# Kernel tuning notes

Measured on AMD Instinct MI355X. Metric: run time of the kernel, lower is better.

Reference implementation:

```python
import math
import jax, jax.numpy as jnp
import numpy as np

B, D, N, K = 16, 512, 2048, 32  # batch, latent_dim, n points, k feature width


def setup_inputs() -> dict:
    key = jax.random.key(0)
    ks = jax.random.split(key, 11)
    s = 0.02
    return {
        "x": jax.random.normal(ks[0], (B, D), jnp.float32),
        "WQ": jax.random.normal(ks[1], (D, N * K), jnp.float32) * s,
        "bQ": jax.random.normal(ks[2], (N * K,), jnp.float32) * s,
        "WK": jax.random.normal(ks[3], (D, N * K), jnp.float32) * s,
        "bK": jax.random.normal(ks[4], (N * K,), jnp.float32) * s,
        "WV": jax.random.normal(ks[5], (D, N * K), jnp.float32) * s,
        "bV": jax.random.normal(ks[6], (N * K,), jnp.float32) * s,
        "Wout": jax.random.normal(ks[7], (3, K), jnp.float32) * s,
        "bout": jax.random.normal(ks[8], (3,), jnp.float32) * s,
        "Wori": jax.random.normal(ks[9], (3, K), jnp.float32) * s,
        "bori": jax.random.normal(ks[10], (3,), jnp.float32) * s,
    }


def reference(x, WQ, bQ, WK, bK, WV, bV, Wout, bout, Wori, bori):
    b = x.shape[0]
    q = (x @ WQ + bQ).reshape(b, N, K)   # fc_Q output, used for both Q and ori
    k = (x @ WK + bK).reshape(b, N, K)
    v = (x @ WV + bV).reshape(b, N, K)
    # conv_ori is a pointwise Conv1d(K, 3, 1) applied to ori^T -> [b,3,N];
    # computed in [b,N,3] layout (final output layout after the last transpose).
    ori = jnp.einsum('bnk,ck->bnc', q, Wori) + bori  # [b, N, 3]
    # single-head scaled dot-product attention, scores [b, N, N]
    scores = jnp.einsum('bnk,bmk->bnm', q, k) / math.sqrt(K)
    attn = jax.nn.softmax(scores, axis=2)
    out = jnp.einsum('bnm,bmk->bnk', attn, v)        # [b, N, K]
    out = jnp.einsum('bnk,ck->bnc', out, Wout) + bout  # pointwise conv_output
    return out + ori                                 # [b, N, 3]
```

## Files before the change

kernel.cpp:

```cpp
#include <hip/hip_runtime.h>
#include <hip/hip_bf16.h>
#include <math.h>

#define NB 16
#define ND 512
#define NN 2048
#define NKF 32
#define NNK 65536

typedef short s8v __attribute__((ext_vector_type(8)));
typedef float f4v __attribute__((ext_vector_type(4)));
typedef unsigned short u16;
typedef unsigned int u32;
typedef u16 u16x8 __attribute__((ext_vector_type(8)));
typedef u32 u32x4 __attribute__((ext_vector_type(4)));

__device__ __forceinline__ u16 f2bf(float x) {
    u32 u = __builtin_bit_cast(u32, x);
    return (u16)((u + 0x7fffu + ((u >> 16) & 1u)) >> 16);
}
__device__ __forceinline__ float bf2f(u16 b) {
    u32 u = ((u32)b) << 16;
    return __builtin_bit_cast(float, u);
}

__global__ __launch_bounds__(256) void proj_partial(
    const float* __restrict__ x,
    const float* __restrict__ WQ, const float* __restrict__ WK,
    const float* __restrict__ WV, u16* __restrict__ part)
{
    const int t = threadIdx.x;
    const int jb = blockIdx.x;
    const int mat = blockIdx.y;
    const int dz = blockIdx.z;
    const float* __restrict__ W = (mat == 0) ? WQ : (mat == 1) ? WK : WV;
    const int j = jb * 1024 + t * 4;
    const int d0 = dz * 128;

    f4v acc[16];
    #pragma unroll
    for (int b = 0; b < 16; b++) acc[b] = (f4v){0.f, 0.f, 0.f, 0.f};

    const float* wp = W + (size_t)d0 * NNK + j;
    const float* xp = x + d0;

    f4v wa[8], wb[8];
    #pragma unroll
    for (int u = 0; u < 8; u++)
        wa[u] = __builtin_nontemporal_load((const f4v*)(wp + (size_t)u * NNK));

    #pragma unroll 1
    for (int dd = 0; dd < 128; dd += 16) {
        #pragma unroll
        for (int u = 0; u < 8; u++)
            wb[u] = __builtin_nontemporal_load(
                (const f4v*)(wp + (size_t)(dd + 8 + u) * NNK));
        __builtin_amdgcn_sched_barrier(0);

        #pragma unroll
        for (int u = 0; u < 8; u++) {
            const float* xr = xp + dd + u;
            #pragma unroll
            for (int b = 0; b < 16; b++) {
                float xv = xr[b * ND];
                acc[b][0] = fmaf(xv, wa[u][0], acc[b][0]);
                acc[b][1] = fmaf(xv, wa[u][1], acc[b][1]);
                acc[b][2] = fmaf(xv, wa[u][2], acc[b][2]);
                acc[b][3] = fmaf(xv, wa[u][3], acc[b][3]);
            }
        }

        if (dd + 16 < 128) {
            #pragma unroll
            for (int u = 0; u < 8; u++)
                wa[u] = __builtin_nontemporal_load(
                    (const f4v*)(wp + (size_t)(dd + 16 + u) * NNK));
        }
        __builtin_amdgcn_sched_barrier(0);

        #pragma unroll
        for (int u = 0; u < 8; u++) {
            const float* xr = xp + dd + 8 + u;
            #pragma unroll
            for (int b = 0; b < 16; b++) {
                float xv = xr[b * ND];
                acc[b][0] = fmaf(xv, wb[u][0], acc[b][0]);
                acc[b][1] = fmaf(xv, wb[u][1], acc[b][1]);
                acc[b][2] = fmaf(xv, wb[u][2], acc[b][2]);
                acc[b][3] = fmaf(xv, wb[u][3], acc[b][3]);
            }
        }
    }

    size_t base = ((size_t)(mat * 4 + dz) * 16) * NNK + j;
    #pragma unroll
    for (int b = 0; b < 16; b++) {
        u32 lo = (u32)f2bf(acc[b][0]) | ((u32)f2bf(acc[b][1]) << 16);
        u32 hi = (u32)f2bf(acc[b][2]) | ((u32)f2bf(acc[b][3]) << 16);
        *(uint2*)(part + base + (size_t)b * NNK) = make_uint2(lo, hi);
    }
}

__global__ __launch_bounds__(256) void reduce_cast(
    const u16* __restrict__ part,
    const float* __restrict__ bQ, const float* __restrict__ bK,
    const float* __restrict__ bV,
    u16* __restrict__ qb, u16* __restrict__ kb, u16* __restrict__ vT)
{
    const int t = threadIdx.x;
    const int jc = blockIdx.x;
    const int b  = blockIdx.y;
    const int mat = blockIdx.z;
    const float* __restrict__ bias = (mat == 0) ? bQ : (mat == 1) ? bK : bV;
    const int j = jc * 2048 + t * 8;

    float4 b0 = *(const float4*)(bias + j);
    float4 b1 = *(const float4*)(bias + j + 4);
    float v[8] = {b0.x, b0.y, b0.z, b0.w, b1.x, b1.y, b1.z, b1.w};

    #pragma unroll
    for (int dz = 0; dz < 4; dz++) {
        size_t p = ((size_t)(mat * 4 + dz) * 16 + b) * NNK + j;
        u16x8 pp = *(const u16x8*)(part + p);
        #pragma unroll
        for (int i = 0; i < 8; i++) v[i] += bf2f(pp[i]);
    }

    const float scale = (mat == 1) ? 0.2550868230023389f : 1.0f;
    u16 h[8];
    #pragma unroll
    for (int i = 0; i < 8; i++) h[i] = f2bf(v[i] * scale);

    __shared__ u16 vt[32][72];

    if (mat < 2) {
        u16* dst = ((mat == 0) ? qb : kb) + (size_t)b * NNK + j;
        u16x8 hv;
        #pragma unroll
        for (int i = 0; i < 8; i++) hv[i] = h[i];
        *(u16x8*)dst = hv;
    } else {
        const int n  = t >> 2;
        const int k0 = (t & 3) * 8;
        #pragma unroll
        for (int i = 0; i < 8; i++) vt[k0 + i][n] = h[i];
        __syncthreads();
        const int k  = t >> 3;
        const int c8 = t & 7;
        u16x8 ov;
        #pragma unroll
        for (int i = 0; i < 8; i++) ov[i] = vt[k][c8 * 8 + i];
        u16* dst = vT + (size_t)b * NNK + (size_t)k * NN + jc * 64 + c8 * 8;
        *(u16x8*)dst = ov;
    }
}

__global__ __launch_bounds__(256) void attn_kernel(
    const u16* __restrict__ qb, const u16* __restrict__ kb,
    const u16* __restrict__ vT,
    const float* __restrict__ Wout, const float* __restrict__ bout,
    const float* __restrict__ Wori, const float* __restrict__ bori,
    float* __restrict__ out)
{
    const int t = threadIdx.x;
    const int w = t >> 6;
    const int l = t & 63;
    const int g = l >> 4;
    const int n = l & 15;
    const int b = blockIdx.y;
    const int q0 = blockIdx.x * 64;

    __shared__ __align__(16) u16 Ks[2][2048];
    __shared__ __align__(16) u16 Vs[2][2048];

    const u16* qrow = qb + (size_t)b * NNK + (size_t)(q0 + w * 16 + n) * NKF + g * 8;
    const s8v qf = *(const s8v*)qrow;

    const int krow = t >> 2, kcol = (t & 3) * 8;
    const int vrow = t >> 3, vslot = t & 7;
    const int vcolL = (vslot ^ (vrow & 7)) * 8;
    const u16* kgp = kb + (size_t)b * NNK + (size_t)krow * NKF + kcol;
    const u16* vgp = vT + (size_t)b * NNK + (size_t)vrow * NN + vcolL;

    s8v kreg, vreg;
    kreg = *(const s8v*)(kgp);                 vreg = *(const s8v*)(vgp);
    *(s8v*)(&Ks[0][t * 8]) = kreg;             *(s8v*)(&Vs[0][t * 8]) = vreg;
    kreg = *(const s8v*)(kgp + (size_t)2048);  vreg = *(const s8v*)(vgp + 64);
    __syncthreads();

    float m_run = -INFINITY, l_run = 0.f;
    f4v O0 = {0.f, 0.f, 0.f, 0.f}, O1 = {0.f, 0.f, 0.f, 0.f};
    const bool hi = (l >= 32);
    const int srcA = ((2 * g) & 3) * 16 + n;
    const int srcB = ((2 * g + 1) & 3) * 16 + n;

    for (int it = 0; it < 32; it++) {
        const int cur = it & 1;
        if (it + 1 < 32) {
            *(s8v*)(&Ks[cur ^ 1][t * 8]) = kreg;
            *(s8v*)(&Vs[cur ^ 1][t * 8]) = vreg;
        }
        if (it + 2 < 32) {
            kreg = *(const s8v*)(kgp + (size_t)(it + 2) * 2048);
            vreg = *(const s8v*)(vgp + (size_t)(it + 2) * 64);
        }

        f4v S[4];
        #pragma unroll
        for (int tt = 0; tt < 4; tt++) {
            s8v ka = *(const s8v*)(&Ks[cur][(n + 16 * tt) * NKF + g * 8]);
            f4v z = {0.f, 0.f, 0.f, 0.f};
            S[tt] = __builtin_amdgcn_mfma_f32_16x16x32_bf16(ka, qf, z, 0, 0, 0);
        }

        float pmax = -INFINITY;
        #pragma unroll
        for (int tt = 0; tt < 4; tt++)
            #pragma unroll
            for (int r = 0; r < 4; r++) pmax = fmaxf(pmax, S[tt][r]);
        pmax = fmaxf(pmax, __shfl_xor(pmax, 16));
        pmax = fmaxf(pmax, __shfl_xor(pmax, 32));
        const float m_new = fmaxf(m_run, pmax);
        const float corr = exp2f(m_run - m_new);

        float p[4][4];
        float tsum = 0.f;
        #pragma unroll
        for (int tt = 0; tt < 4; tt++)
            #pragma unroll
            for (int r = 0; r < 4; r++) {
                p[tt][r] = exp2f(S[tt][r] - m_new);
                tsum += p[tt][r];
            }
        tsum += __shfl_xor(tsum, 16);
        tsum += __shfl_xor(tsum, 32);
        l_run = l_run * corr + tsum;
        m_run = m_new;
        #pragma unroll
        for (int r = 0; r < 4; r++) { O0[r] *= corr; O1[r] *= corr; }

        u32 pk[4][2];
        #pragma unroll
        for (int tt = 0; tt < 4; tt++) {
            pk[tt][0] = (u32)f2bf(p[tt][0]) | ((u32)f2bf(p[tt][1]) << 16);
            pk[tt][1] = (u32)f2bf(p[tt][2]) | ((u32)f2bf(p[tt][3]) << 16);
        }

        #pragma unroll
        for (int kc = 0; kc < 2; kc++) {
            u32 lo0 = (u32)__shfl((int)pk[2 * kc][0], srcA);
            u32 hi0 = (u32)__shfl((int)pk[2 * kc + 1][0], srcA);
            u32 lo1 = (u32)__shfl((int)pk[2 * kc][1], srcA);
            u32 hi1 = (u32)__shfl((int)pk[2 * kc + 1][1], srcA);
            u32 lo2 = (u32)__shfl((int)pk[2 * kc][0], srcB);
            u32 hi2 = (u32)__shfl((int)pk[2 * kc + 1][0], srcB);
            u32 lo3 = (u32)__shfl((int)pk[2 * kc][1], srcB);
            u32 hi3 = (u32)__shfl((int)pk[2 * kc + 1][1], srcB);
            u32x4 fr;
            fr.x = hi ? hi0 : lo0;
            fr.y = hi ? hi1 : lo1;
            fr.z = hi ? hi2 : lo2;
            fr.w = hi ? hi3 : lo3;
            s8v pa = __builtin_bit_cast(s8v, fr);

            {
                int row = n;
                int slot = (g + 4 * kc) ^ (row & 7);
                s8v va = *(const s8v*)(&Vs[cur][row * 64 + slot * 8]);
                O0 = __builtin_amdgcn_mfma_f32_16x16x32_bf16(va, pa, O0, 0, 0, 0);
            }
            {
                int row = n + 16;
                int slot = (g + 4 * kc) ^ (row & 7);
                s8v va = *(const s8v*)(&Vs[cur][row * 64 + slot * 8]);
                O1 = __builtin_amdgcn_mfma_f32_16x16x32_bf16(va, pa, O1, 0, 0, 0);
            }
        }
        __syncthreads();
    }

    const float inv = 1.0f / l_run;
    float po[3] = {0.f, 0.f, 0.f};
    #pragma unroll
    for (int r = 0; r < 4; r++) {
        int dk0 = 4 * g + r;
        int dk1 = 16 + 4 * g + r;
        float o0 = O0[r] * inv;
        float o1 = O1[r] * inv;
        #pragma unroll
        for (int c = 0; c < 3; c++) {
            po[c] += o0 * Wout[c * NKF + dk0];
            po[c] += o1 * Wout[c * NKF + dk1];
        }
    }
    #pragma unroll
    for (int e = 0; e < 8; e++) {
        float qv = bf2f((u16)qf[e]);
        int k = 8 * g + e;
        #pragma unroll
        for (int c = 0; c < 3; c++) po[c] += qv * Wori[c * NKF + k];
    }
    #pragma unroll
    for (int c = 0; c < 3; c++) {
        po[c] += __shfl_xor(po[c], 16);
        po[c] += __shfl_xor(po[c], 32);
    }
    if (g == 0) {
        int row = q0 + w * 16 + n;
        size_t o = ((size_t)b * NN + row) * 3;
        #pragma unroll
        for (int c = 0; c < 3; c++) out[o + c] = po[c] + bout[c] + bori[c];
    }
}

extern "C" void kernel_launch(void* const* d_in, const int* in_sizes, int n_in,
                              void* d_out, int out_size, void* d_ws, size_t ws_size,
                              hipStream_t stream) {
    const float* x    = (const float*)d_in[0];
    const float* WQ   = (const float*)d_in[1];
    const float* bQ   = (const float*)d_in[2];
    const float* WK   = (const float*)d_in[3];
    const float* bK   = (const float*)d_in[4];
    const float* WV   = (const float*)d_in[5];
    const float* bV   = (const float*)d_in[6];
    const float* Wout = (const float*)d_in[7];
    const float* bout = (const float*)d_in[8];
    const float* Wori = (const float*)d_in[9];
    const float* bori = (const float*)d_in[10];
    float* out = (float*)d_out;

    char* ws = (char*)d_ws;
    u16* part = (u16*)ws;
    u16* qb = (u16*)(ws + 25165824);
    u16* kb = (u16*)(ws + 25165824 + 2097152);
    u16* vT = (u16*)(ws + 25165824 + 2 * 2097152);

    proj_partial<<<dim3(64, 3, 4), 256, 0, stream>>>(x, WQ, WK, WV, part);
    reduce_cast<<<dim3(32, 16, 3), 256, 0, stream>>>(part, bQ, bK, bV, qb, kb, vT);
    attn_kernel<<<dim3(32, 16), 256, 0, stream>>>(qb, kb, vT, Wout, bout, Wori, bori, out);
}
```

Measured before the change: 133.6 us.

## Load K fragments directly to registers and exchange P through LDS

K tiles are now read straight from global memory into MFMA operand registers, double-buffered across iterations, instead of being staged through shared memory. The P matrix transpose between the two MFMAs now goes through a small per-wave LDS buffer rather than eight cross-lane shuffles with selects. The loop is manually unrolled by two so the K register buffers can swap roles. This removes LDS traffic and a sync dependency for K and cuts shuffle work, but issues more, smaller global loads per thread and adds LDS writes and reads for P.

After: 132.6 us. No clear change (-0.7%).

```diff
diff --git a/kernel.cpp b/kernel.cpp
--- a/kernel.cpp
+++ b/kernel.cpp
@@ -170,47 +170,47 @@
     const int b = blockIdx.y;
     const int q0 = blockIdx.x * 64;
 
-    __shared__ __align__(16) u16 Ks[2][2048];
     __shared__ __align__(16) u16 Vs[2][2048];
+    __shared__ __align__(16) u32 Pt[4][16][36];
 
     const u16* qrow = qb + (size_t)b * NNK + (size_t)(q0 + w * 16 + n) * NKF + g * 8;
     const s8v qf = *(const s8v*)qrow;
 
-    const int krow = t >> 2, kcol = (t & 3) * 8;
+    const u16* kbase = kb + (size_t)b * NNK + (size_t)n * NKF + g * 8;
+    auto loadK = [&](s8v (&ka)[4], int it) {
+        #pragma unroll
+        for (int tt = 0; tt < 4; tt++)
+            ka[tt] = *(const s8v*)(kbase + (size_t)it * 2048 + tt * 512);
+    };
+
     const int vrow = t >> 3, vslot = t & 7;
     const int vcolL = (vslot ^ (vrow & 7)) * 8;
-    const u16* kgp = kb + (size_t)b * NNK + (size_t)krow * NKF + kcol;
     const u16* vgp = vT + (size_t)b * NNK + (size_t)vrow * NN + vcolL;
 
-    s8v kreg, vreg;
-    kreg = *(const s8v*)(kgp);                 vreg = *(const s8v*)(vgp);
-    *(s8v*)(&Ks[0][t * 8]) = kreg;             *(s8v*)(&Vs[0][t * 8]) = vreg;
-    kreg = *(const s8v*)(kgp + (size_t)2048);  vreg = *(const s8v*)(vgp + 64);
+    s8v ka0[4], ka1[4], vreg;
+    loadK(ka0, 0);
+    vreg = *(const s8v*)(vgp);
+    *(s8v*)(&Vs[0][t * 8]) = vreg;
+    vreg = *(const s8v*)(vgp + 64);
     __syncthreads();
 
     float m_run = -INFINITY, l_run = 0.f;
     f4v O0 = {0.f, 0.f, 0.f, 0.f}, O1 = {0.f, 0.f, 0.f, 0.f};
-    const bool hi = (l >= 32);
-    const int srcA = ((2 * g) & 3) * 16 + n;
-    const int srcB = ((2 * g + 1) & 3) * 16 + n;
-
-    for (int it = 0; it < 32; it++) {
+
+    auto body = [&](s8v (&kc_)[4], s8v (&kn_)[4], int it) {
         const int cur = it & 1;
         if (it + 1 < 32) {
-            *(s8v*)(&Ks[cur ^ 1][t * 8]) = kreg;
             *(s8v*)(&Vs[cur ^ 1][t * 8]) = vreg;
-        }
-        if (it + 2 < 32) {
-            kreg = *(const s8v*)(kgp + (size_t)(it + 2) * 2048);
+            loadK(kn_, it + 1);
+        }
+        if (it + 2 < 32)
             vreg = *(const s8v*)(vgp + (size_t)(it + 2) * 64);
-        }
 
         f4v S[4];
         #pragma unroll
         for (int tt = 0; tt < 4; tt++) {
-            s8v ka = *(const s8v*)(&Ks[cur][(n + 16 * tt) * NKF + g * 8]);
             f4v z = {0.f, 0.f, 0.f, 0.f};
-            S[tt] = __builtin_amdgcn_mfma_f32_16x16x32_bf16(ka, qf, z, 0, 0, 0);
+            S[tt] = __builtin_amdgcn_mfma_f32_16x16x32_bf16(kc_[tt], qf, z, 0, 0, 0);
         }
 
         float pmax = -INFINITY;
@@ -239,30 +239,17 @@
         #pragma unroll
         for (int r = 0; r < 4; r++) { O0[r] *= corr; O1[r] *= corr; }
 
-        u32 pk[4][2];
         #pragma unroll
         for (int tt = 0; tt < 4; tt++) {
-            pk[tt][0] = (u32)f2bf(p[tt][0]) | ((u32)f2bf(p[tt][1]) << 16);
-            pk[tt][1] = (u32)f2bf(p[tt][2]) | ((u32)f2bf(p[tt][3]) << 16);
+            u32 w0 = (u32)f2bf(p[tt][0]) | ((u32)f2bf(p[tt][1]) << 16);
+            u32 w1 = (u32)f2bf(p[tt][2]) | ((u32)f2bf(p[tt][3]) << 16);
+            *(uint2*)&Pt[w][n][8 * tt + 2 * g] = make_uint2(w0, w1);
         }
 
         #pragma unroll
         for (int kc = 0; kc < 2; kc++) {
-            u32 lo0 = (u32)__shfl((int)pk[2 * kc][0], srcA);
-            u32 hi0 = (u32)__shfl((int)pk[2 * kc + 1][0], srcA);
-            u32 lo1 = (u32)__shfl((int)pk[2 * kc][1], srcA);
-            u32 hi1 = (u32)__shfl((int)pk[2 * kc + 1][1], srcA);
-            u32 lo2 = (u32)__shfl((int)pk[2 * kc][0], srcB);
-            u32 hi2 = (u32)__shfl((int)pk[2 * kc + 1][0], srcB);
-            u32 lo3 = (u32)__shfl((int)pk[2 * kc][1], srcB);
-            u32 hi3 = (u32)__shfl((int)pk[2 * kc + 1][1], srcB);
-            u32x4 fr;
-            fr.x = hi ? hi0 : lo0;
-            fr.y = hi ? hi1 : lo1;
-            fr.z = hi ? hi2 : lo2;
-            fr.w = hi ? hi3 : lo3;
-            s8v pa = __builtin_bit_cast(s8v, fr);
-
+            u32x4 pw = *(const u32x4*)&Pt[w][n][16 * kc + 4 * g];
+            s8v pa = __builtin_bit_cast(s8v, pw);
             {
                 int row = n;
                 int slot = (g + 4 * kc) ^ (row & 7);
@@ -277,6 +264,12 @@
             }
         }
         __syncthreads();
+    };
+
+    #pragma unroll 1
+    for (int i2 = 0; i2 < 16; i2++) {
+        body(ka0, ka1, 2 * i2);
+        body(ka1, ka0, 2 * i2 + 1);
     }
 
     const float inv = 1.0f / l_run;
```
